# Kernel optimization log

Measured on AMD Instinct MI355X. Metric: run time of the kernel, lower is better.

The kernel has to match this reference:

```python
import jax, jax.numpy as jnp
import numpy as np

B, L, F2, T, D, H = 128, 196, 512, 32, 256, 512


def setup_inputs() -> dict:
    key = jax.random.key(0)
    ks = jax.random.split(key, 12)
    g = lambda k, sh, s: (jax.random.normal(k, sh, dtype=jnp.float32) * s)
    return {
        "input_data": g(ks[0], (B, L, F2), 1.0),
        "word_inputs": g(ks[1], (B, T, D), 1.0),
        # init-state projections (glorot-ish scale)
        "w_h": g(ks[2], (F2, H), 0.04),
        "b_h": jnp.zeros((H,), jnp.float32),
        "w_c": g(ks[3], (F2, H), 0.04),
        "b_c": jnp.zeros((H,), jnp.float32),
        # simple additive attention (L2Attention=False, Gatted=False)
        "w_a_h": g(ks[4], (H, 1), 0.06),
        "w_a": g(ks[5], (F2, 1), 0.06),
        "b_a": jnp.zeros((1,), jnp.float32),
        # keras LSTMCell params: kernel [D+F2, 4H], recurrent [H, 4H], bias [4H]
        "lstm_kernel": g(ks[6], (D + F2, 4 * H), 0.03),
        "lstm_recurrent": g(ks[7], (H, 4 * H), 0.03),
        "lstm_bias": jnp.zeros((4 * H,), jnp.float32),
    }


def reference(input_data, word_inputs, w_h, b_h, w_c, b_c, w_a_h, w_a, b_a,
              lstm_kernel, lstm_recurrent, lstm_bias):
    # initial states from mean-pooled features
    features_mean = jnp.mean(input_data, axis=1)          # [B, F2]
    h = jnp.tanh(features_mean @ w_h + b_h)               # [B, H]
    c = jnp.tanh(features_mean @ w_c + b_c)               # [B, H]

    # time-invariant part of the attention score: input_data @ w_a -> [B, L]
    feat_score = jnp.einsum('blf,fo->blo', input_data, w_a)[..., 0] + b_a[0]

    def step(carry, word_t):
        h, c = carry
        # additive attention: tanh(h@w_a_h [B,1] + feat_score [B,L]) -> softmax over L
        score = jnp.tanh((h @ w_a_h) + feat_score)        # [B, L]
        alfa = jax.nn.softmax(score, axis=-1)             # [B, L]
        context = jnp.einsum('blf,bl->bf', input_data, alfa)  # [B, F2]
        # keras LSTMCell: gate order i, f, g(cell), o
        x = jnp.concatenate([word_t, context], axis=1)    # [B, D+F2]
        z = x @ lstm_kernel + h @ lstm_recurrent + lstm_bias
        i, f, g, o = jnp.split(z, 4, axis=-1)
        c_new = jax.nn.sigmoid(f) * c + jax.nn.sigmoid(i) * jnp.tanh(g)
        h_new = jax.nn.sigmoid(o) * jnp.tanh(c_new)
        return (h_new, c_new), (h_new, c_new, alfa)

    (_, _), (hs, cs, alfas) = jax.lax.scan(step, (h, c), jnp.swapaxes(word_inputs, 0, 1))
    hiddens = jnp.swapaxes(hs, 0, 1)   # [B, T, H]
    memory = cs                        # [T, B, H] (original returns a list of T [B,H] tensors)
    alfas = jnp.swapaxes(alfas, 0, 1)  # [B, T, L]
    return hiddens, memory, alfas
```

## Files before the change

### kernel.cpp

```cpp
#include <hip/hip_runtime.h>
#include <math.h>

#define B  128
#define L  196
#define F2 512
#define T  32
#define D  256
#define H  512
#define H4 2048
#define KCAT 1280
#define KS 4
#define KCHUNK 320

typedef __attribute__((ext_vector_type(8))) short bf16x8;
typedef __attribute__((ext_vector_type(4))) float f32x4;

__device__ __forceinline__ float sigf(float x) { return 1.0f / (1.0f + expf(-x)); }
__device__ __forceinline__ unsigned short f2bf(float x) {
    unsigned u = __float_as_uint(x);
    u += 0x7FFF + ((u >> 16) & 1);
    return (unsigned short)(u >> 16);
}
__device__ __forceinline__ float bf2f(unsigned short s) {
    return __uint_as_float(((unsigned)s) << 16);
}
__device__ __forceinline__ float wred_sum(float v) {
    for (int o = 32; o > 0; o >>= 1) v += __shfl_down(v, o);
    return v;
}


__global__ void k_prep2(const float* __restrict__ X, const float* __restrict__ w_a,
                        const float* __restrict__ b_a, unsigned short* __restrict__ Xb,
                        float* __restrict__ fscore, float* __restrict__ fmpart) {
    __shared__ float sp[8][512];
    int b = blockIdx.x, g = blockIdx.y, tid = threadIdx.x;
    int rowi = tid >> 5, lane32 = tid & 31;
    int f0 = tid * 2;
    float2 acc = make_float2(0.f, 0.f);
    for (int s = 0; s < 4; ++s) {
        int li = s * 8 + rowi;
        float4 part[4];
        if (li < 28) {
            size_t row = (size_t)b * L + g * 28 + li;
            const float* src = X + row * F2;
            unsigned short* dst = Xb + row * F2;
            float sc = 0.f;
            #pragma unroll
            for (int j = 0; j < 4; ++j) {
                int f = j * 128 + lane32 * 4;
                float4 v = *(const float4*)(src + f);
                float4 w = *(const float4*)(w_a + f);
                sc += v.x * w.x + v.y * w.y + v.z * w.z + v.w * w.w;
                part[j] = v;
                ushort4 u;
                u.x = f2bf(v.x); u.y = f2bf(v.y); u.z = f2bf(v.z); u.w = f2bf(v.w);
                *(ushort4*)(dst + f) = u;
            }
            for (int o = 16; o > 0; o >>= 1) sc += __shfl_down(sc, o, 32);
            if (lane32 == 0) fscore[row] = sc + b_a[0];
        } else {
            #pragma unroll
            for (int j = 0; j < 4; ++j) part[j] = make_float4(0.f, 0.f, 0.f, 0.f);
        }
        __syncthreads();
        #pragma unroll
        for (int j = 0; j < 4; ++j)
            *(float4*)&sp[rowi][j * 128 + lane32 * 4] = part[j];
        __syncthreads();
        #pragma unroll
        for (int r = 0; r < 8; ++r) { acc.x += sp[r][f0]; acc.y += sp[r][f0 + 1]; }
    }
    *(float2*)&fmpart[((size_t)b * 7 + g) * 512 + f0] = acc;
}

__global__ void k_mred(const float* __restrict__ fmpart, unsigned short* __restrict__ fmb) {
    int b = blockIdx.x, tid = threadIdx.x;
    int f0 = tid * 2;
    float2 acc = make_float2(0.f, 0.f);
    #pragma unroll
    for (int g = 0; g < 7; ++g) {
        float2 v = *(const float2*)&fmpart[((size_t)b * 7 + g) * 512 + f0];
        acc.x += v.x; acc.y += v.y;
    }
    ushort2 u; u.x = f2bf(acc.x * (1.0f / L)); u.y = f2bf(acc.y * (1.0f / L));
    *(ushort2*)(fmb + (size_t)b * F2 + f0) = u;
}

__global__ void k_castw(const float* __restrict__ src, unsigned short* __restrict__ dst) {
    size_t i = ((size_t)blockIdx.x * 256 + threadIdx.x) * 8;
    float4 v0 = *(const float4*)(src + i);
    float4 v1 = *(const float4*)(src + i + 4);
    ushort4 u0, u1;
    u0.x = f2bf(v0.x); u0.y = f2bf(v0.y); u0.z = f2bf(v0.z); u0.w = f2bf(v0.w);
    u1.x = f2bf(v1.x); u1.y = f2bf(v1.y); u1.z = f2bf(v1.z); u1.w = f2bf(v1.w);
    *(ushort4*)(dst + i) = u0;
    *(ushort4*)(dst + i + 4) = u1;
}

__global__ void k_trW(const float* __restrict__ k_w, const float* __restrict__ r_w,
                      unsigned short* __restrict__ WcatT) {
    int job = blockIdx.z;
    if (job == 2 && blockIdx.x >= 8) return;
    const float* src; int colOff;
    if (job == 0)      { src = k_w + (size_t)256 * H4; colOff = 0; }
    else if (job == 1) { src = r_w;                    colOff = 512; }
    else               { src = k_w;                    colOff = 1024; }
    __shared__ float Ls[32][65];
    int r0 = blockIdx.x * 32, c0 = blockIdx.y * 64;
    int tid = threadIdx.x;
    int r = tid >> 3, c8 = (tid & 7) * 8;
    const float* s = src + (size_t)(r0 + r) * H4 + c0 + c8;
    #pragma unroll
    for (int j = 0; j < 8; ++j) Ls[r][c8 + j] = s[j];
    __syncthreads();
    int cc = tid >> 2, q = tid & 3;
    unsigned short tmp[8];
    #pragma unroll
    for (int j = 0; j < 8; ++j) tmp[j] = f2bf(Ls[q * 8 + j][cc]);
    *(float4*)(WcatT + (size_t)(c0 + cc) * KCAT + colOff + r0 + q * 8) = *(float4*)tmp;
}

__global__ void k_trI(const float* __restrict__ w_h, const float* __restrict__ w_c,
                      unsigned short* __restrict__ wiT) {
    int job = blockIdx.z;
    const float* src = job ? w_c : w_h;
    unsigned short* dst = wiT + (size_t)job * 512 * 512;
    __shared__ float Ls[32][65];
    int r0 = blockIdx.x * 32, c0 = blockIdx.y * 64;
    int tid = threadIdx.x;
    int r = tid >> 3, c8 = (tid & 7) * 8;
    const float* s = src + (size_t)(r0 + r) * 512 + c0 + c8;
    #pragma unroll
    for (int j = 0; j < 8; ++j) Ls[r][c8 + j] = s[j];
    __syncthreads();
    int cc = tid >> 2, q = tid & 3;
    unsigned short tmp[8];
    #pragma unroll
    for (int j = 0; j < 8; ++j) tmp[j] = f2bf(Ls[q * 8 + j][cc]);
    *(float4*)(dst + (size_t)(c0 + cc) * 512 + r0 + q * 8) = *(float4*)tmp;
}

__global__ __launch_bounds__(256) void k_init_gemm(
    const unsigned short* __restrict__ A, const unsigned short* __restrict__ Bt,
    const float* __restrict__ b_h, const float* __restrict__ b_c,
    unsigned short* __restrict__ Abuf0, float* __restrict__ cbuf) {
    __shared__ short As[128 * 64];
    __shared__ short Bs[128 * 64];
    int tid = threadIdx.x;
    int nbase = blockIdx.x * 128;
    int wave = tid >> 6, lane = tid & 63;
    int wm = (wave >> 1) * 64, wn = (wave & 1) * 64;
    int l15 = lane & 15, l4 = lane >> 4;

    f32x4 acc[4][4];
    #pragma unroll
    for (int i = 0; i < 4; ++i)
        #pragma unroll
        for (int j = 0; j < 4; ++j) acc[i][j] = (f32x4){0.f, 0.f, 0.f, 0.f};

    for (int it = 0; it < 8; ++it) {
        int kbase = it * 64;
        #pragma unroll
        for (int ch = 0; ch < 4; ++ch) {
            int idx = ch * 256 + tid;
            int row = idx >> 3, q = idx & 7;
            int k = kbase + q * 8;
            float4 v = *(const float4*)(A + (size_t)row * 512 + k);
            *(float4*)&As[row * 64 + ((q ^ (row & 7)) << 3)] = v;
            float4 w = *(const float4*)(Bt + (size_t)(nbase + row) * 512 + k);
            *(float4*)&Bs[row * 64 + ((q ^ (row & 7)) << 3)] = w;
        }
        __syncthreads();
        #pragma unroll
        for (int ks = 0; ks < 2; ++ks) {
            bf16x8 a[4], b[4];
            #pragma unroll
            for (int f = 0; f < 4; ++f) {
                int ar = wm + f * 16 + l15;
                int q = ks * 4 + l4;
                a[f] = *(const bf16x8*)&As[ar * 64 + ((q ^ (ar & 7)) << 3)];
                int br = wn + f * 16 + l15;
                b[f] = *(const bf16x8*)&Bs[br * 64 + ((q ^ (br & 7)) << 3)];
            }
            #pragma unroll
            for (int fm = 0; fm < 4; ++fm)
                #pragma unroll
                for (int fn = 0; fn < 4; ++fn)
                    acc[fm][fn] = __builtin_amdgcn_mfma_f32_16x16x32_bf16(a[fm], b[fn], acc[fm][fn], 0, 0, 0);
        }
        __syncthreads();
    }
    #pragma unroll
    for (int fm = 0; fm < 4; ++fm)
        #pragma unroll
        for (int j = 0; j < 4; ++j) {
            int m = wm + fm * 16 + l4 * 4 + j;
            #pragma unroll
            for (int fn = 0; fn < 4; ++fn) {
                int gn = nbase + wn + fn * 16 + l15;
                float v = acc[fm][fn][j];
                if (gn < 512) Abuf0[(size_t)m * 1024 + 512 + gn] = f2bf(tanhf(v + b_h[gn]));
                else          cbuf[(size_t)m * 512 + gn - 512] = tanhf(v + b_c[gn - 512]);
            }
        }
}

__global__ __launch_bounds__(256) void k_gemm32(
    const unsigned short* __restrict__ Abuf, const unsigned short* __restrict__ wordb,
    const unsigned short* __restrict__ WcatT, float* __restrict__ zpart, int t) {
    __shared__ short As[64 * 64];
    __shared__ short Bs[32 * 64];
    int tid = threadIdx.x;
    int bid = blockIdx.x;
    int ksb = bid >> 7, rem = bid & 127;
    int rowbase = (rem >> 6) * 64, nbase = (rem & 63) * 32;
    int wave = tid >> 6, lane = tid & 63;
    int wm = (wave & 1) * 32, wn = (wave >> 1) * 16;
    int l15 = lane & 15, l4 = lane >> 4;

    f32x4 acc[2];
    acc[0] = (f32x4){0.f, 0.f, 0.f, 0.f};
    acc[1] = (f32x4){0.f, 0.f, 0.f, 0.f};

    for (int it = 0; it < KCHUNK / 64; ++it) {
        int kbase = ksb * KCHUNK + it * 64;
        #pragma unroll
        for (int p = 0; p < 2; ++p) {
            int idx = p * 256 + tid;
            int row = idx >> 3, q = idx & 7;
            int k = kbase + q * 8;
            int gr = rowbase + row;
            float4 v;
            if (k < 1024) v = *(const float4*)(Abuf + (size_t)gr * 1024 + k);
            else          v = *(const float4*)(wordb + ((size_t)gr * T + t) * D + (k - 1024));
            *(float4*)&As[row * 64 + ((q ^ (row & 7)) << 3)] = v;
        }
        {
            int row = tid >> 3, q = tid & 7;
            float4 w = *(const float4*)(WcatT + (size_t)(nbase + row) * KCAT + kbase + q * 8);
            *(float4*)&Bs[row * 64 + ((q ^ (row & 7)) << 3)] = w;
        }
        __syncthreads();
        #pragma unroll
        for (int ks2 = 0; ks2 < 2; ++ks2) {
            int q = ks2 * 4 + l4;
            bf16x8 a[2], bb;
            #pragma unroll
            for (int fm = 0; fm < 2; ++fm) {
                int ar = wm + fm * 16 + l15;
                a[fm] = *(const bf16x8*)&As[ar * 64 + ((q ^ (ar & 7)) << 3)];
            }
            {
                int br = wn + l15;
                bb = *(const bf16x8*)&Bs[br * 64 + ((q ^ (br & 7)) << 3)];
            }
            #pragma unroll
            for (int fm = 0; fm < 2; ++fm)
                acc[fm] = __builtin_amdgcn_mfma_f32_16x16x32_bf16(a[fm], bb, acc[fm], 0, 0, 0);
        }
        __syncthreads();
    }
    float* zp = zpart + (size_t)ksb * B * H4;
    #pragma unroll
    for (int fm = 0; fm < 2; ++fm)
        #pragma unroll
        for (int j = 0; j < 4; ++j) {
            int m = rowbase + wm + fm * 16 + l4 * 4 + j;
            zp[(size_t)m * H4 + nbase + wn + l15] = acc[fm][j];
        }
}

__global__ __launch_bounds__(256) void k_step4(
    const float* __restrict__ zpart, const float* __restrict__ bias,
    const float* __restrict__ cb_cur, float* __restrict__ cb_nxt,
    unsigned short* __restrict__ Abuf,
    const unsigned short* __restrict__ Xb, const float* __restrict__ fscore,
    const float* __restrict__ w_a_h,
    float* __restrict__ out_h, float* __restrict__ out_m, float* __restrict__ out_a,
    int t_next) {
    __shared__ float red[8];
    __shared__ float sal[200];
    __shared__ float sp2[4][64][2];
    int b = blockIdx.x, quarter = blockIdx.y, tid = threadIdx.x;
    int lane = tid & 63, wid = tid >> 6;
    int n0 = tid * 2;
    float hp;
    if (t_next > 0) {
        float2 z[4];
        #pragma unroll
        for (int g = 0; g < 4; ++g) z[g] = *(const float2*)(bias + g * H + n0);
        #pragma unroll
        for (int ks = 0; ks < KS; ++ks) {
            const float* zp = zpart + ((size_t)ks * B + b) * H4;
            #pragma unroll
            for (int g = 0; g < 4; ++g) {
                float2 v = *(const float2*)(zp + g * H + n0);
                z[g].x += v.x; z[g].y += v.y;
            }
        }
        float2 cv = *(const float2*)(cb_cur + (size_t)b * H + n0);
        float cnx = sigf(z[1].x) * cv.x + sigf(z[0].x) * tanhf(z[2].x);
        float cny = sigf(z[1].y) * cv.y + sigf(z[0].y) * tanhf(z[2].y);
        float hnx = sigf(z[3].x) * tanhf(cnx);
        float hny = sigf(z[3].y) * tanhf(cny);
        if (quarter == 0) {
            int tp = t_next - 1;
            *(float2*)(cb_nxt + (size_t)b * H + n0) = make_float2(cnx, cny);
            *(float2*)(out_m + ((size_t)tp * B + b) * H + n0) = make_float2(cnx, cny);
            *(float2*)(out_h + ((size_t)b * T + tp) * H + n0) = make_float2(hnx, hny);
            ushort2 hu; hu.x = f2bf(hnx); hu.y = f2bf(hny);
            *(ushort2*)(Abuf + (size_t)b * 1024 + 512 + n0) = hu;
        }
        hp = hnx * w_a_h[n0] + hny * w_a_h[n0 + 1];
    } else {
        ushort2 hu = *(const ushort2*)(Abuf + (size_t)b * 1024 + 512 + n0);
        hp = bf2f(hu.x) * w_a_h[n0] + bf2f(hu.y) * w_a_h[n0 + 1];
    }
    if (t_next >= T) return;

    float s = wred_sum(hp);
    if (lane == 0) red[wid] = s;
    __syncthreads();
    float hs = red[0] + red[1] + red[2] + red[3];
    float scv = (tid < L) ? tanhf(hs + fscore[b * L + tid]) : 0.f;
    float ex = (tid < L) ? expf(scv) : 0.f;
    float es = wred_sum(ex);
    if (lane == 0) red[4 + wid] = es;
    __syncthreads();
    float denom = red[4] + red[5] + red[6] + red[7];
    float al = ex / denom;
    if (tid < L) {
        sal[tid] = al;
        if (quarter == 0) out_a[((size_t)b * T + t_next) * L + tid] = al;
    }
    __syncthreads();

    int fi = tid & 63, lg = tid >> 6;
    const unsigned* xb32 = (const unsigned*)(Xb + (size_t)b * L * F2) + quarter * 64 + fi;
    int l0 = lg * 49;
    float a0 = 0.f, a1 = 0.f;
    for (int sblk = 0; sblk < 49; sblk += 7) {
        unsigned u[7];
        #pragma unroll
        for (int j = 0; j < 7; ++j) u[j] = xb32[(size_t)(l0 + sblk + j) * 256];
        #pragma unroll
        for (int j = 0; j < 7; ++j) {
            float w = sal[l0 + sblk + j];
            a0 += bf2f((unsigned short)(u[j] & 0xFFFF)) * w;
            a1 += bf2f((unsigned short)(u[j] >> 16)) * w;
        }
    }
    sp2[lg][fi][0] = a0; sp2[lg][fi][1] = a1;
    __syncthreads();
    if (tid < 64) {
        ushort2 cu;
        cu.x = f2bf(sp2[0][tid][0] + sp2[1][tid][0] + sp2[2][tid][0] + sp2[3][tid][0]);
        cu.y = f2bf(sp2[0][tid][1] + sp2[1][tid][1] + sp2[2][tid][1] + sp2[3][tid][1]);
        *(ushort2*)(Abuf + (size_t)b * 1024 + (quarter * 64 + tid) * 2) = cu;
    }
}

extern "C" void kernel_launch(void* const* d_in, const int* in_sizes, int n_in,
                              void* d_out, int out_size, void* d_ws, size_t ws_size,
                              hipStream_t stream) {
    (void)in_sizes; (void)n_in; (void)out_size; (void)ws_size;
    const float* X     = (const float*)d_in[0];
    const float* word  = (const float*)d_in[1];
    const float* w_h   = (const float*)d_in[2];
    const float* b_h   = (const float*)d_in[3];
    const float* w_c   = (const float*)d_in[4];
    const float* b_c   = (const float*)d_in[5];
    const float* w_a_h = (const float*)d_in[6];
    const float* w_a   = (const float*)d_in[7];
    const float* b_a   = (const float*)d_in[8];
    const float* k_w   = (const float*)d_in[9];
    const float* r_w   = (const float*)d_in[10];
    const float* bias  = (const float*)d_in[11];

    float* out_h = (float*)d_out;
    float* out_m = out_h + (size_t)B * T * H;
    float* out_a = out_m + (size_t)T * B * H;

    char* p = (char*)d_ws;
    unsigned short* Xb    = (unsigned short*)p; p += (size_t)B * L * F2 * 2;
    unsigned short* WcatT = (unsigned short*)p; p += (size_t)H4 * KCAT * 2;
    unsigned short* wiT   = (unsigned short*)p; p += (size_t)1024 * 512 * 2;
    unsigned short* wordb = (unsigned short*)p; p += (size_t)B * T * D * 2;
    unsigned short* fmb   = (unsigned short*)p; p += (size_t)B * F2 * 2;
    unsigned short* Abuf  = (unsigned short*)p; p += (size_t)B * 1024 * 2;
    float* fscore = (float*)p; p += (size_t)B * L * 4;
    float* cb0    = (float*)p; p += (size_t)B * H * 4;
    float* cb1    = (float*)p; p += (size_t)B * H * 4;
    float* zpart  = (float*)p; p += (size_t)KS * B * H4 * 4;
    float* fmpart = zpart;

    k_prep2<<<dim3(B, 7), 256, 0, stream>>>(X, w_a, b_a, Xb, fscore, fmpart);
    k_mred<<<B, 256, 0, stream>>>(fmpart, fmb);
    k_castw<<<512, 256, 0, stream>>>(word, wordb);
    k_trW<<<dim3(16, 32, 3), 256, 0, stream>>>(k_w, r_w, WcatT);
    k_trI<<<dim3(16, 8, 2), 256, 0, stream>>>(w_h, w_c, wiT);
    k_init_gemm<<<8, 256, 0, stream>>>(fmb, wiT, b_h, b_c, Abuf, cb0);

    float* cb[2] = {cb0, cb1};
    k_step4<<<dim3(B, 4), 256, 0, stream>>>(zpart, bias, cb0, cb1, Abuf, Xb,
                                            fscore, w_a_h, out_h, out_m, out_a, 0);
    for (int t = 0; t < T; ++t) {
        k_gemm32<<<512, 256, 0, stream>>>(Abuf, wordb, WcatT, zpart, t);
        k_step4<<<dim3(B, 4), 256, 0, stream>>>(zpart, bias, cb[t & 1], cb[(t + 1) & 1],
                                                Abuf, Xb, fscore, w_a_h,
                                                out_h, out_m, out_a, t + 1);
    }
}
```

Baseline: 510.7 us.

## Hoist word-input projection out of recurrence into one batched GEMM

```diff
diff --git a/kernel.cpp b/kernel.cpp
--- a/kernel.cpp
+++ b/kernel.cpp
@@ -8,9 +8,9 @@
 #define D  256
 #define H  512
 #define H4 2048
-#define KCAT 1280
+#define KCAT 1024
 #define KS 4
-#define KCHUNK 320
+#define KCHUNK 256
 
 typedef __attribute__((ext_vector_type(8))) short bf16x8;
 typedef __attribute__((ext_vector_type(4))) float f32x4;
@@ -87,25 +87,14 @@
     *(ushort2*)(fmb + (size_t)b * F2 + f0) = u;
 }
 
-__global__ void k_castw(const float* __restrict__ src, unsigned short* __restrict__ dst) {
-    size_t i = ((size_t)blockIdx.x * 256 + threadIdx.x) * 8;
-    float4 v0 = *(const float4*)(src + i);
-    float4 v1 = *(const float4*)(src + i + 4);
-    ushort4 u0, u1;
-    u0.x = f2bf(v0.x); u0.y = f2bf(v0.y); u0.z = f2bf(v0.z); u0.w = f2bf(v0.w);
-    u1.x = f2bf(v1.x); u1.y = f2bf(v1.y); u1.z = f2bf(v1.z); u1.w = f2bf(v1.w);
-    *(ushort4*)(dst + i) = u0;
-    *(ushort4*)(dst + i + 4) = u1;
-}
-
 __global__ void k_trW(const float* __restrict__ k_w, const float* __restrict__ r_w,
-                      unsigned short* __restrict__ WcatT) {
+                      unsigned short* __restrict__ WcatT, unsigned short* __restrict__ wT) {
     int job = blockIdx.z;
     if (job == 2 && blockIdx.x >= 8) return;
-    const float* src; int colOff;
-    if (job == 0)      { src = k_w + (size_t)256 * H4; colOff = 0; }
-    else if (job == 1) { src = r_w;                    colOff = 512; }
-    else               { src = k_w;                    colOff = 1024; }
+    const float* src; unsigned short* dstBase; int dstLD, colOff;
+    if (job == 0)      { src = k_w + (size_t)256 * H4; dstBase = WcatT; dstLD = KCAT; colOff = 0; }
+    else if (job == 1) { src = r_w;                    dstBase = WcatT; dstLD = KCAT; colOff = 512; }
+    else               { src = k_w;                    dstBase = wT;    dstLD = 256;  colOff = 0; }
     __shared__ float Ls[32][65];
     int r0 = blockIdx.x * 32, c0 = blockIdx.y * 64;
     int tid = threadIdx.x;
@@ -118,7 +107,7 @@
     unsigned short tmp[8];
     #pragma unroll
     for (int j = 0; j < 8; ++j) tmp[j] = f2bf(Ls[q * 8 + j][cc]);
-    *(float4*)(WcatT + (size_t)(c0 + cc) * KCAT + colOff + r0 + q * 8) = *(float4*)tmp;
+    *(float4*)(dstBase + (size_t)(c0 + cc) * dstLD + colOff + r0 + q * 8) = *(float4*)tmp;
 }
 
 __global__ void k_trI(const float* __restrict__ w_h, const float* __restrict__ w_c,
@@ -206,9 +195,77 @@
         }
 }
 
+__global__ __launch_bounds__(256) void k_wgemm(
+    const float* __restrict__ word,
+    const unsigned short* __restrict__ wT,
+    float* __restrict__ wpart) {
+    __shared__ short As[128 * 64];
+    __shared__ short Bs[128 * 64];
+    int tid = threadIdx.x;
+    int nbase = blockIdx.x * 128;
+    int mbase = blockIdx.y * 128;
+    int wave = tid >> 6, lane = tid & 63;
+    int wm = (wave >> 1) * 64, wn = (wave & 1) * 64;
+    int l15 = lane & 15, l4 = lane >> 4;
+
+    f32x4 acc[4][4];
+    #pragma unroll
+    for (int i = 0; i < 4; ++i)
+        #pragma unroll
+        for (int j = 0; j < 4; ++j) acc[i][j] = (f32x4){0.f, 0.f, 0.f, 0.f};
+
+    for (int it = 0; it < 4; ++it) {
+        int kbase = it * 64;
+        #pragma unroll
+        for (int ch = 0; ch < 4; ++ch) {
+            int idx = ch * 256 + tid;
+            int row = idx >> 3, q = idx & 7;
+            int k = kbase + q * 8;
+            const float* ap = word + (size_t)(mbase + row) * 256 + k;
+            float4 v0 = *(const float4*)ap;
+            float4 v1 = *(const float4*)(ap + 4);
+            unsigned short tmp[8];
+            tmp[0] = f2bf(v0.x); tmp[1] = f2bf(v0.y); tmp[2] = f2bf(v0.z); tmp[3] = f2bf(v0.w);
+            tmp[4] = f2bf(v1.x); tmp[5] = f2bf(v1.y); tmp[6] = f2bf(v1.z); tmp[7] = f2bf(v1.w);
+            *(float4*)&As[row * 64 + ((q ^ (row & 7)) << 3)] = *(float4*)tmp;
+            float4 w = *(const float4*)(wT + (size_t)(nbase + row) * 256 + k);
+            *(float4*)&Bs[row * 64 + ((q ^ (row & 7)) << 3)] = w;
+        }
+        __syncthreads();
+        #pragma unroll
+        for (int ks = 0; ks < 2; ++ks) {
+            bf16x8 a[4], b[4];
+            #pragma unroll
+            for (int f = 0; f < 4; ++f) {
+                int ar = wm + f * 16 + l15;
+                int q = ks * 4 + l4;
+                a[f] = *(const bf16x8*)&As[ar * 64 + ((q ^ (ar & 7)) << 3)];
+                int br = wn + f * 16 + l15;
+                b[f] = *(const bf16x8*)&Bs[br * 64 + ((q ^ (br & 7)) << 3)];
+            }
+            #pragma unroll
+            for (int fm = 0; fm < 4; ++fm)
+                #pragma unroll
+                for (int fn = 0; fn < 4; ++fn)
+                    acc[fm][fn] = __builtin_amdgcn_mfma_f32_16x16x32_bf16(a[fm], b[fn], acc[fm][fn], 0, 0, 0);
+        }
+        __syncthreads();
+    }
+    #pragma unroll
+    for (int fm = 0; fm < 4; ++fm)
+        #pragma unroll
+        for (int j = 0; j < 4; ++j) {
+            int m = wm + fm * 16 + l4 * 4 + j;
+            #pragma unroll
+            for (int fn = 0; fn < 4; ++fn)
+                wpart[(size_t)(mbase + m) * H4 + nbase + wn + fn * 16 + l15] = acc[fm][fn][j];
+        }
+}
+
 __global__ __launch_bounds__(256) void k_gemm32(
-    const unsigned short* __restrict__ Abuf, const unsigned short* __restrict__ wordb,
-    const unsigned short* __restrict__ WcatT, float* __restrict__ zpart, int t) {
+    const unsigned short* __restrict__ Abuf,
+    const unsigned short* __restrict__ WcatT,
+    float* __restrict__ zpart) {
     __shared__ short As[64 * 64];
     __shared__ short Bs[32 * 64];
     int tid = threadIdx.x;
@@ -230,10 +287,7 @@
             int idx = p * 256 + tid;
             int row = idx >> 3, q = idx & 7;
             int k = kbase + q * 8;
-            int gr = rowbase + row;
-            float4 v;
-            if (k < 1024) v = *(const float4*)(Abuf + (size_t)gr * 1024 + k);
-            else          v = *(const float4*)(wordb + ((size_t)gr * T + t) * D + (k - 1024));
+            float4 v = *(const float4*)(Abuf + (size_t)(rowbase + row) * 1024 + k);
             *(float4*)&As[row * 64 + ((q ^ (row & 7)) << 3)] = v;
         }
         {
@@ -272,7 +326,8 @@
 }
 
 __global__ __launch_bounds__(256) void k_step4(
-    const float* __restrict__ zpart, const float* __restrict__ bias,
+    const float* __restrict__ zpart, const float* __restrict__ wpart,
+    const float* __restrict__ bias,
     const float* __restrict__ cb_cur, float* __restrict__ cb_nxt,
     unsigned short* __restrict__ Abuf,
     const unsigned short* __restrict__ Xb, const float* __restrict__ fscore,
@@ -287,9 +342,14 @@
     int n0 = tid * 2;
     float hp;
     if (t_next > 0) {
+        const float* wp = wpart + ((size_t)b * T + (t_next - 1)) * H4;
         float2 z[4];
         #pragma unroll
-        for (int g = 0; g < 4; ++g) z[g] = *(const float2*)(bias + g * H + n0);
+        for (int g = 0; g < 4; ++g) {
+            float2 bz = *(const float2*)(bias + g * H + n0);
+            float2 wz = *(const float2*)(wp + g * H + n0);
+            z[g].x = bz.x + wz.x; z[g].y = bz.y + wz.y;
+        }
         #pragma unroll
         for (int ks = 0; ks < KS; ++ks) {
             const float* zp = zpart + ((size_t)ks * B + b) * H4;
@@ -385,29 +445,30 @@
     char* p = (char*)d_ws;
     unsigned short* Xb    = (unsigned short*)p; p += (size_t)B * L * F2 * 2;
     unsigned short* WcatT = (unsigned short*)p; p += (size_t)H4 * KCAT * 2;
+    unsigned short* wT    = (unsigned short*)p; p += (size_t)H4 * 256 * 2;
     unsigned short* wiT   = (unsigned short*)p; p += (size_t)1024 * 512 * 2;
-    unsigned short* wordb = (unsigned short*)p; p += (size_t)B * T * D * 2;
     unsigned short* fmb   = (unsigned short*)p; p += (size_t)B * F2 * 2;
     unsigned short* Abuf  = (unsigned short*)p; p += (size_t)B * 1024 * 2;
     float* fscore = (float*)p; p += (size_t)B * L * 4;
     float* cb0    = (float*)p; p += (size_t)B * H * 4;
     float* cb1    = (float*)p; p += (size_t)B * H * 4;
     float* zpart  = (float*)p; p += (size_t)KS * B * H4 * 4;
+    float* wpart  = (float*)p; p += (size_t)B * T * H4 * 4;
     float* fmpart = zpart;
 
     k_prep2<<<dim3(B, 7), 256, 0, stream>>>(X, w_a, b_a, Xb, fscore, fmpart);
     k_mred<<<B, 256, 0, stream>>>(fmpart, fmb);
-    k_castw<<<512, 256, 0, stream>>>(word, wordb);
-    k_trW<<<dim3(16, 32, 3), 256, 0, stream>>>(k_w, r_w, WcatT);
+    k_trW<<<dim3(16, 32, 3), 256, 0, stream>>>(k_w, r_w, WcatT, wT);
     k_trI<<<dim3(16, 8, 2), 256, 0, stream>>>(w_h, w_c, wiT);
+    k_wgemm<<<dim3(16, 32), 256, 0, stream>>>(word, wT, wpart);
     k_init_gemm<<<8, 256, 0, stream>>>(fmb, wiT, b_h, b_c, Abuf, cb0);
 
     float* cb[2] = {cb0, cb1};
-    k_step4<<<dim3(B, 4), 256, 0, stream>>>(zpart, bias, cb0, cb1, Abuf, Xb,
+    k_step4<<<dim3(B, 4), 256, 0, stream>>>(zpart, wpart, bias, cb0, cb1, Abuf, Xb,
                                             fscore, w_a_h, out_h, out_m, out_a, 0);
     for (int t = 0; t < T; ++t) {
-        k_gemm32<<<512, 256, 0, stream>>>(Abuf, wordb, WcatT, zpart, t);
-        k_step4<<<dim3(B, 4), 256, 0, stream>>>(zpart, bias, cb[t & 1], cb[(t + 1) & 1],
+        k_gemm32<<<512, 256, 0, stream>>>(Abuf, WcatT, zpart);
+        k_step4<<<dim3(B, 4), 256, 0, stream>>>(zpart, wpart, bias, cb[t & 1], cb[(t + 1) & 1],
                                                 Abuf, Xb, fscore, w_a_h,
                                                 out_h, out_m, out_a, t + 1);
     }
```

New measurement: 461.2 us. 9.7% less time.
